# Kernel optimization log

Hardware: AMD Instinct MI355X
Metric: run time of the kernel (lower is better)

## Reference

```python
import jax, jax.numpy as jnp
import numpy as np

B, S, D, H, OUT = 64, 2048, 1024, 300, 2
DROPOUT = 0.2


def setup_inputs() -> dict:
    key = jax.random.key(0)
    k_in, k_ids, k_pos, k_mask, k_w1, k_w2 = jax.random.split(key, 6)
    inputs = jax.random.normal(k_in, (B, S, D), dtype=jnp.float32)
    # token ids in [2, 32000); then plant a single '1' (EOS/pad marker) per row
    input_ids = jax.random.randint(k_ids, (B, S), 2, 32000, dtype=jnp.int64)
    eos_pos = jax.random.randint(k_pos, (B,), S // 2, S)
    input_ids = input_ids.at[jnp.arange(B), eos_pos].set(1)
    # realized Bernoulli(1 - dropout) token-keep mask, [B, S, 1]
    drop_mask = (jax.random.uniform(k_mask, (B, S, 1)) < (1.0 - DROPOUT)).astype(jnp.float32)
    W1 = jax.random.normal(k_w1, (H, D), dtype=jnp.float32) * 0.02
    b1 = jnp.zeros((H,), dtype=jnp.float32)
    W2 = jax.random.normal(k_w2, (OUT, H), dtype=jnp.float32) * 0.02
    b2 = jnp.zeros((OUT,), dtype=jnp.float32)
    return {"inputs": inputs, "input_ids": input_ids, "drop_mask": drop_mask,
            "W1": W1, "b1": b1, "W2": W2, "b2": b2}


def reference(inputs, input_ids, drop_mask, W1, b1, W2, b2):
    # end_ind[i] = first position where input_ids[i] == 1; fallback matches
    # the original's `except: end_ind = input_ids.shape[0]` (== batch size)
    is_end = input_ids == 1                              # [B, S]
    has_end = jnp.any(is_end, axis=1)                    # [B]
    first_end = jnp.argmax(is_end, axis=1)               # [B]
    end_ind = jnp.where(has_end, first_end, input_ids.shape[0])

    # masked, dropped segment-average over the first end_ind tokens
    valid = (jnp.arange(inputs.shape[1])[None, :] < end_ind[:, None])  # [B, S]
    weighted = inputs * drop_mask * valid[:, :, None].astype(inputs.dtype)
    euph = weighted.sum(axis=1) / end_ind[:, None].astype(inputs.dtype)  # [B, D]

    # 2-layer MLP with tanh
    hidden = jnp.tanh(euph @ W1.T + b1)
    out = hidden @ W2.T + b2                             # [B, 2]
    return out
```

## Files before the change

### kernel.cpp

```cpp
#include <hip/hip_runtime.h>
#include <math.h>

#define B 64
#define S 2048
#define D 1024
#define H 300
#define NOUT 2
#define NCHUNK 16
#define CHUNK_S (S / NCHUNK)

typedef float fx4 __attribute__((ext_vector_type(4)));

static __device__ __forceinline__ int imin(int a, int b) { return a < b ? a : b; }

__global__ __launch_bounds__(256) void end_kernel(const int* __restrict__ ids,
                                                  int* __restrict__ end_ind) {
    int b = blockIdx.x;
    int t = threadIdx.x;
    const int* row = ids + (size_t)b * S;
    int m = S;
    for (int s = t; s < S; s += 256) {
        if (row[s] == 1 && s < m) m = s;
    }
    __shared__ int red[256];
    red[t] = m;
    __syncthreads();
    for (int st = 128; st > 0; st >>= 1) {
        if (t < st) red[t] = imin(red[t], red[t + st]);
        __syncthreads();
    }
    if (t == 0) end_ind[b] = (red[0] < S) ? red[0] : B;
}

__global__ __launch_bounds__(256) void sum_partial_kernel(
        const float* __restrict__ inputs,
        const float* __restrict__ drop,
        const int* __restrict__ end_ind,
        float* __restrict__ partial ) {
    int chunk = blockIdx.x;
    int b = blockIdx.y;
    int t = threadIdx.x;
    int e = end_ind[b];
    int s0 = chunk * CHUNK_S;
    int s1 = imin(s0 + CHUNK_S, e);
    int n = s1 - s0;

    fx4 a0 = (fx4)(0.f);
    fx4 a1 = a0, a2 = a0, a3 = a0;
    __shared__ float w_lds[CHUNK_S];

    if (n > 0) {
        if (t < CHUNK_S) {
            w_lds[t] = (t < n) ? drop[(size_t)b * S + s0 + t] : 0.f;
        }
        __syncthreads();
        const fx4* p = (const fx4*)(inputs + ((size_t)b * S + s0) * D) + t;
        const int R = D / 4;
        int i = 0;
        for (; i + 4 <= n; i += 4, p += 4 * R) {
            fx4 v0 = __builtin_nontemporal_load(p + 0 * R);
            fx4 v1 = __builtin_nontemporal_load(p + 1 * R);
            fx4 v2 = __builtin_nontemporal_load(p + 2 * R);
            fx4 v3 = __builtin_nontemporal_load(p + 3 * R);
            a0 += v0 * w_lds[i + 0];
            a1 += v1 * w_lds[i + 1];
            a2 += v2 * w_lds[i + 2];
            a3 += v3 * w_lds[i + 3];
        }
        for (; i < n; ++i, p += R) {
            fx4 v = __builtin_nontemporal_load(p);
            a0 += v * w_lds[i];
        }
        a0 += (a1 + a2) + a3;
    }
    fx4* op = (fx4*)(partial + ((size_t)b * NCHUNK + chunk) * D) + t;
    *op = a0;
}

__global__ __launch_bounds__(256) void mlp_kernel(
        const float* __restrict__ partial,
        const int* __restrict__ end_ind,
        const float* __restrict__ W1, const float* __restrict__ b1,
        const float* __restrict__ W2, const float* __restrict__ b2,
        float* __restrict__ out) {
    int b = blockIdx.x;
    int t = threadIdx.x;
    __shared__ fx4 x4[D / 4];
    __shared__ float hidden[H];
    __shared__ float red[256];

    float inv_e = 1.0f / (float)end_ind[b];
    {
        fx4 a = (fx4)(0.f);
        const fx4* p = (const fx4*)(partial + (size_t)b * NCHUNK * D) + t;
        for (int c = 0; c < NCHUNK; ++c, p += D / 4) {
            a += p[0];
        }
        x4[t] = a * inv_e;
    }
    __syncthreads();

    for (int h = t; h < H; h += 256) {
        const fx4* w = (const fx4*)(W1 + (size_t)h * D);
        fx4 acc = (fx4)(0.f);
        for (int k = 0; k < D / 4; ++k) {
            acc += x4[k] * w[k];
        }
        hidden[h] = tanhf(acc.x + acc.y + acc.z + acc.w + b1[h]);
    }
    __syncthreads();

    for (int o = 0; o < NOUT; ++o) {
        float p = 0.f;
        for (int h = t; h < H; h += 256) p += hidden[h] * W2[(size_t)o * H + h];
        red[t] = p;
        __syncthreads();
        for (int st = 128; st > 0; st >>= 1) {
            if (t < st) red[t] += red[t + st];
            __syncthreads();
        }
        if (t == 0) out[b * NOUT + o] = red[0] + b2[o];
        __syncthreads();
    }
}

extern "C" void kernel_launch(void* const* d_in, const int* in_sizes, int n_in,
                              void* d_out, int out_size, void* d_ws, size_t ws_size,
                              hipStream_t stream) {
    const float* inputs = (const float*)d_in[0];
    const int*   ids    = (const int*)d_in[1];
    const float* drop   = (const float*)d_in[2];
    const float* W1     = (const float*)d_in[3];
    const float* b1v    = (const float*)d_in[4];
    const float* W2     = (const float*)d_in[5];
    const float* b2v    = (const float*)d_in[6];
    float* out = (float*)d_out;

    int*   end_ind = (int*)d_ws;
    float* partial = (float*)((char*)d_ws + 256);

    end_kernel<<<B, 256, 0, stream>>>(ids, end_ind);
    sum_partial_kernel<<<dim3(NCHUNK, B), 256, 0, stream>>>(inputs, drop, end_ind, partial);
    mlp_kernel<<<B, 256, 0, stream>>>(partial, end_ind, W1, b1v, W2, b2v, out);
}
```

Measured before the change: 695.0 us.

## Skip dropped rows via ballot compaction and parallelize MLP dot products across waves

The partial-sum kernel now compacts the non-zero dropout weights in each chunk into a row list using a wave ballot. It then loads only the kept rows, which avoids reading the roughly 20% of input rows whose weight is zero. NCHUNK doubles to 32 for more blocks, and the main loop unrolls to 8 accumulators with regular loads instead of nontemporal ones. The MLP kernel switches from one thread per hidden unit with serial dot products to one wave per hidden unit with coalesced W1 reads and a shuffle reduction, in exchange for more partial buffers to reduce.

```diff
diff --git a/kernel.cpp b/kernel.cpp
--- a/kernel.cpp
+++ b/kernel.cpp
@@ -6,7 +6,7 @@
 #define D 1024
 #define H 300
 #define NOUT 2
-#define NCHUNK 16
+#define NCHUNK 32
 #define CHUNK_S (S / NCHUNK)
 
 typedef float fx4 __attribute__((ext_vector_type(4)));
@@ -40,39 +40,56 @@
     int chunk = blockIdx.x;
     int b = blockIdx.y;
     int t = threadIdx.x;
+
+    __shared__ int   rows_l[CHUNK_S];
+    __shared__ float w_l[CHUNK_S];
+    __shared__ int   cnt_l;
+
     int e = end_ind[b];
     int s0 = chunk * CHUNK_S;
-    int s1 = imin(s0 + CHUNK_S, e);
-    int n = s1 - s0;
+    int n = imin(s0 + CHUNK_S, e) - s0;
 
+    if (t < 64) {
+        float w = 0.f;
+        if (t < n) w = drop[(size_t)b * S + s0 + t];
+        unsigned long long mask = __ballot(w != 0.f);
+        int pos = __popcll(mask & ((1ull << t) - 1ull));
+        if (w != 0.f) { rows_l[pos] = t; w_l[pos] = w; }
+        if (t == 0) cnt_l = __popcll(mask);
+    }
+    __syncthreads();
+
+    int m = cnt_l;
     fx4 a0 = (fx4)(0.f);
-    fx4 a1 = a0, a2 = a0, a3 = a0;
-    __shared__ float w_lds[CHUNK_S];
+    fx4 a1 = a0, a2 = a0, a3 = a0, a4 = a0, a5 = a0, a6 = a0, a7 = a0;
 
-    if (n > 0) {
-        if (t < CHUNK_S) {
-            w_lds[t] = (t < n) ? drop[(size_t)b * S + s0 + t] : 0.f;
-        }
-        __syncthreads();
-        const fx4* p = (const fx4*)(inputs + ((size_t)b * S + s0) * D) + t;
-        const int R = D / 4;
-        int i = 0;
-        for (; i + 4 <= n; i += 4, p += 4 * R) {
-            fx4 v0 = __builtin_nontemporal_load(p + 0 * R);
-            fx4 v1 = __builtin_nontemporal_load(p + 1 * R);
-            fx4 v2 = __builtin_nontemporal_load(p + 2 * R);
-            fx4 v3 = __builtin_nontemporal_load(p + 3 * R);
-            a0 += v0 * w_lds[i + 0];
-            a1 += v1 * w_lds[i + 1];
-            a2 += v2 * w_lds[i + 2];
-            a3 += v3 * w_lds[i + 3];
-        }
-        for (; i < n; ++i, p += R) {
-            fx4 v = __builtin_nontemporal_load(p);
-            a0 += v * w_lds[i];
-        }
-        a0 += (a1 + a2) + a3;
+    const char* base = (const char*)inputs + (((size_t)b * S + s0) * D + 4 * (size_t)t) * sizeof(float);
+
+    int i = 0;
+    for (; i + 8 <= m; i += 8) {
+        fx4 v0 = *(const fx4*)(base + ((size_t)rows_l[i + 0] << 12));
+        fx4 v1 = *(const fx4*)(base + ((size_t)rows_l[i + 1] << 12));
+        fx4 v2 = *(const fx4*)(base + ((size_t)rows_l[i + 2] << 12));
+        fx4 v3 = *(const fx4*)(base + ((size_t)rows_l[i + 3] << 12));
+        fx4 v4 = *(const fx4*)(base + ((size_t)rows_l[i + 4] << 12));
+        fx4 v5 = *(const fx4*)(base + ((size_t)rows_l[i + 5] << 12));
+        fx4 v6 = *(const fx4*)(base + ((size_t)rows_l[i + 6] << 12));
+        fx4 v7 = *(const fx4*)(base + ((size_t)rows_l[i + 7] << 12));
+        a0 += v0 * w_l[i + 0];
+        a1 += v1 * w_l[i + 1];
+        a2 += v2 * w_l[i + 2];
+        a3 += v3 * w_l[i + 3];
+        a4 += v4 * w_l[i + 4];
+        a5 += v5 * w_l[i + 5];
+        a6 += v6 * w_l[i + 6];
+        a7 += v7 * w_l[i + 7];
     }
+    for (; i < m; ++i) {
+        fx4 v = *(const fx4*)(base + ((size_t)rows_l[i] << 12));
+        a0 += v * w_l[i];
+    }
+    a0 = ((a0 + a1) + (a2 + a3)) + ((a4 + a5) + (a6 + a7));
+
     fx4* op = (fx4*)(partial + ((size_t)b * NCHUNK + chunk) * D) + t;
     *op = a0;
 }
@@ -85,6 +102,9 @@
         float* __restrict__ out) {
     int b = blockIdx.x;
     int t = threadIdx.x;
+    int wave = t >> 6;
+    int lane = t & 63;
+
     __shared__ fx4 x4[D / 4];
     __shared__ float hidden[H];
     __shared__ float red[256];
@@ -100,13 +120,21 @@
     }
     __syncthreads();
 
-    for (int h = t; h < H; h += 256) {
+    fx4 xr0 = x4[lane];
+    fx4 xr1 = x4[lane + 64];
+    fx4 xr2 = x4[lane + 128];
+    fx4 xr3 = x4[lane + 192];
+
+    for (int h = wave; h < H; h += 4) {
         const fx4* w = (const fx4*)(W1 + (size_t)h * D);
-        fx4 acc = (fx4)(0.f);
-        for (int k = 0; k < D / 4; ++k) {
-            acc += x4[k] * w[k];
-        }
-        hidden[h] = tanhf(acc.x + acc.y + acc.z + acc.w + b1[h]);
+        fx4 acc = xr0 * w[lane]
+                + xr1 * w[lane + 64]
+                + xr2 * w[lane + 128]
+                + xr3 * w[lane + 192];
+        float d = acc.x + acc.y + acc.z + acc.w;
+        #pragma unroll
+        for (int mm = 32; mm > 0; mm >>= 1) d += __shfl_xor(d, mm, 64);
+        if (lane == 0) hidden[h] = tanhf(d + b1[h]);
     }
     __syncthreads();
 
```

Result: slower. 733.2 us (+5.5%).
